# Kernel optimization log

Hardware: AMD Instinct MI355X
Metric: run time of the kernel (lower is better)

Reference implementation:

```python
import jax, jax.numpy as jnp
import numpy as np
from jax import lax

# BinarizedConv2d (threshold=False branch): per-direction binary conv.
# Bits {0,1} map to {-1,+1}; output = 2*A - K where A = #bit-agreements
# between the patch and the filter, K = Cin*kH*kW (the 'offset').
# A = 2*sum(x&w) - sum(x) - sum(w) + K  =>  out = 4*xw - 2*sx - 2*sw + K.

D, H, W, CIN = 64, 32, 32, 128
KH = KW = 3
COUT = 128
PAD = 1


def _binconv(x, w):
    # x: [D,H,W,Cin] bool, w: [D,kH,kW,Cin,Cout] with 0/1 float values
    d, h, wd, c = x.shape
    kh, kw, cout = w.shape[1], w.shape[2], w.shape[4]
    K = c * kh * kw  # offset = in_channels * kH * kW
    xf = jnp.transpose(x.astype(w.dtype), (0, 3, 1, 2))  # [D,C,H,W]
    # im2col: [D, C*kH*kW, Ho, Wo], feature index = c*kH*kW + i*kW + j
    patches = lax.conv_general_dilated_patches(
        xf, (kh, kw), (1, 1), [(PAD, PAD), (PAD, PAD)])
    ho, wo = patches.shape[2], patches.shape[3]
    p = patches.reshape(d, c, kh, kw, ho, wo)
    xw = jnp.einsum('dcijhw,dijco->dhwo', p, w)      # sum(x & w)
    sx = p.sum(axis=(1, 2, 3))                        # [D,Ho,Wo]
    sw = w.sum(axis=(1, 2, 3))                        # [D,Cout]
    return 4.0 * xw - 2.0 * sx[..., None] - 2.0 * sw[:, None, None, :] + K


def setup_inputs() -> dict:
    key = jax.random.key(0)
    kx, kw = jax.random.split(key)
    x = jax.random.bernoulli(kx, 0.5, (D, H, W, CIN))
    w = jax.random.bernoulli(kw, 0.5, (D, KH, KW, CIN, COUT)).astype(jnp.float32)
    return {'x': x, 'w': w}


def reference(x, w):
    return _binconv(x, w)  # [D,Ho,Wo,Cout] signed binary conv values
```

## Files before the change

kernel.cpp:

```cpp
#include <hip/hip_runtime.h>
#include <hip/hip_bf16.h>
#include <stdint.h>


#define D_    64
#define H_    32
#define W_    32
#define CIN_  128
#define COUT_ 128
#define KK_   1152

__global__ __launch_bounds__(256) void pack_x_kernel(const int* __restrict__ x,
                                                     uint4* __restrict__ xb) {
    int gid = blockIdx.x * 256 + threadIdx.x;
    int pos = gid >> 5;
    int c4  = gid & 31;
    const int4* xp = (const int4*)(x + (long)pos * CIN_) + c4;
    int4 v = *xp;
    unsigned long long b0 = __ballot(v.x != 0);
    unsigned long long b1 = __ballot(v.y != 0);
    unsigned long long b2 = __ballot(v.z != 0);
    unsigned long long b3 = __ballot(v.w != 0);
    int lane = threadIdx.x & 63;
    if (lane == 0)
        xb[pos] = make_uint4((unsigned)b0, (unsigned)b1, (unsigned)b2, (unsigned)b3);
    else if (lane == 32)
        xb[pos] = make_uint4((unsigned)(b0 >> 32), (unsigned)(b1 >> 32),
                             (unsigned)(b2 >> 32), (unsigned)(b3 >> 32));
}

__global__ __launch_bounds__(256) void pack_w_kernel(const float* __restrict__ w,
                                                     unsigned* __restrict__ wb) {
    int t    = blockIdx.x * 256 + threadIdx.x;
    int o    = t & 127;
    int rest = t >> 7;
    int k    = rest & 3;
    int dt   = rest >> 2;
    int d    = dt / 9;
    int tap  = dt - d * 9;
    const float* wp = w + (long)dt * (CIN_ * COUT_) + o;
    unsigned m = 0;
#pragma unroll
    for (int j = 0; j < 32; ++j) {
        if (wp[(long)(4 * j + k) * COUT_] != 0.f) m |= 1u << j;
    }
    wb[(((long)d * COUT_ + o) * 9 + tap) * 4 + k] = m;
}

__global__ __launch_bounds__(256) void binconv_kernel(const uint4* __restrict__ xb,
                                                      const uint4* __restrict__ wb,
                                                      float* __restrict__ out) {
    __shared__ uint4 xbt[4][34];

    int bid  = blockIdx.x;
    int d    = bid >> 4;
    int tile = bid & 15;
    int h0   = tile * 2;
    int tid  = threadIdx.x;
    int o    = tid & 127;
    int grp  = tid >> 7;

    if (tid < 4 * 34) {
        int r  = tid / 34;
        int cc = tid - r * 34;
        int hh = h0 - 1 + r;
        int ww = cc - 1;
        uint4 v = make_uint4(0u, 0u, 0u, 0u);
        if (hh >= 0 && hh < H_ && ww >= 0 && ww < W_)
            v = xb[(long)d * (H_ * W_) + hh * W_ + ww];
        xbt[r][cc] = v;
    }

    uint4 wv[9];
    const uint4* wp = wb + (long)(d * COUT_ + o) * 9;
#pragma unroll
    for (int t = 0; t < 9; ++t) wv[t] = wp[t];

    __syncthreads();

    int h = h0 + grp;
    float* op = out + ((long)d * (H_ * W_) + h * W_) * COUT_ + o;

    uint4 ca[3], cb[3], cc_[3];
#pragma unroll
    for (int i = 0; i < 3; ++i) {
        ca[i] = xbt[grp + i][0];
        cb[i] = xbt[grp + i][1];
    }

#pragma unroll
    for (int iw = 0; iw < W_; ++iw) {
#pragma unroll
        for (int i = 0; i < 3; ++i) cc_[i] = xbt[grp + i][iw + 2];
        int pop = 0;
#pragma unroll
        for (int i = 0; i < 3; ++i) {
            uint4 xa;
            uint4 w0 = wv[i * 3 + 0], w1 = wv[i * 3 + 1], w2 = wv[i * 3 + 2];
            xa = ca[i];
            pop += __popc(xa.x ^ w0.x) + __popc(xa.y ^ w0.y)
                 + __popc(xa.z ^ w0.z) + __popc(xa.w ^ w0.w);
            xa = cb[i];
            pop += __popc(xa.x ^ w1.x) + __popc(xa.y ^ w1.y)
                 + __popc(xa.z ^ w1.z) + __popc(xa.w ^ w1.w);
            xa = cc_[i];
            pop += __popc(xa.x ^ w2.x) + __popc(xa.y ^ w2.y)
                 + __popc(xa.z ^ w2.z) + __popc(xa.w ^ w2.w);
        }
        op[(long)iw * COUT_] = (float)(KK_ - 2 * pop);
#pragma unroll
        for (int i = 0; i < 3; ++i) { ca[i] = cb[i]; cb[i] = cc_[i]; }
    }
}

extern "C" void kernel_launch(void* const* d_in, const int* in_sizes, int n_in,
                              void* d_out, int out_size, void* d_ws, size_t ws_size,
                              hipStream_t stream) {
    const int*   x   = (const int*)d_in[0];
    const float* w   = (const float*)d_in[1];
    float*       out = (float*)d_out;

    uint4*    xb = (uint4*)d_ws;
    unsigned* wb = (unsigned*)(xb + (D_ * H_ * W_));

    pack_x_kernel<<<8192, 256, 0, stream>>>(x, xb);
    pack_w_kernel<<<1152, 256, 0, stream>>>(w, wb);
    binconv_kernel<<<1024, 256, 0, stream>>>(xb, (const uint4*)wb, out);
}
```

Before: 128.5 us.

## Fuse x/w bit-packing and binary conv into one kernel

```diff
diff --git a/kernel.cpp b/kernel.cpp
--- a/kernel.cpp
+++ b/kernel.cpp
@@ -1,5 +1,4 @@
 #include <hip/hip_runtime.h>
-#include <hip/hip_bf16.h>
 #include <stdint.h>
 
 
@@ -10,73 +9,71 @@
 #define COUT_ 128
 #define KK_   1152
 
-__global__ __launch_bounds__(256) void pack_x_kernel(const int* __restrict__ x,
-                                                     uint4* __restrict__ xb) {
-    int gid = blockIdx.x * 256 + threadIdx.x;
-    int pos = gid >> 5;
-    int c4  = gid & 31;
-    const int4* xp = (const int4*)(x + (long)pos * CIN_) + c4;
-    int4 v = *xp;
-    unsigned long long b0 = __ballot(v.x != 0);
-    unsigned long long b1 = __ballot(v.y != 0);
-    unsigned long long b2 = __ballot(v.z != 0);
-    unsigned long long b3 = __ballot(v.w != 0);
-    int lane = threadIdx.x & 63;
-    if (lane == 0)
-        xb[pos] = make_uint4((unsigned)b0, (unsigned)b1, (unsigned)b2, (unsigned)b3);
-    else if (lane == 32)
-        xb[pos] = make_uint4((unsigned)(b0 >> 32), (unsigned)(b1 >> 32),
-                             (unsigned)(b2 >> 32), (unsigned)(b3 >> 32));
-}
+__global__ __launch_bounds__(1024) void fused_kernel(const int* __restrict__ x,
+                                                     const float* __restrict__ w,
+                                                     float* __restrict__ out) {
+    __shared__ uint4    xbt[10][34];
+    __shared__ unsigned wt[128][40];
 
-__global__ __launch_bounds__(256) void pack_w_kernel(const float* __restrict__ w,
-                                                     unsigned* __restrict__ wb) {
-    int t    = blockIdx.x * 256 + threadIdx.x;
-    int o    = t & 127;
-    int rest = t >> 7;
-    int k    = rest & 3;
-    int dt   = rest >> 2;
-    int d    = dt / 9;
-    int tap  = dt - d * 9;
-    const float* wp = w + (long)dt * (CIN_ * COUT_) + o;
-    unsigned m = 0;
-#pragma unroll
-    for (int j = 0; j < 32; ++j) {
-        if (wp[(long)(4 * j + k) * COUT_] != 0.f) m |= 1u << j;
-    }
-    wb[(((long)d * COUT_ + o) * 9 + tap) * 4 + k] = m;
-}
+    int tid  = threadIdx.x;
+    int bid  = blockIdx.x;
+    int d    = bid & 63;
+    int tile = bid >> 6;
+    int h0   = tile * 8;
 
-__global__ __launch_bounds__(256) void binconv_kernel(const uint4* __restrict__ xb,
-                                                      const uint4* __restrict__ wb,
-                                                      float* __restrict__ out) {
-    __shared__ uint4 xbt[4][34];
-
-    int bid  = blockIdx.x;
-    int d    = bid >> 4;
-    int tile = bid & 15;
-    int h0   = tile * 2;
-    int tid  = threadIdx.x;
-    int o    = tid & 127;
-    int grp  = tid >> 7;
-
-    if (tid < 4 * 34) {
-        int r  = tid / 34;
-        int cc = tid - r * 34;
-        int hh = h0 - 1 + r;
-        int ww = cc - 1;
-        uint4 v = make_uint4(0u, 0u, 0u, 0u);
-        if (hh >= 0 && hh < H_ && ww >= 0 && ww < W_)
-            v = xb[(long)d * (H_ * W_) + hh * W_ + ww];
-        xbt[r][cc] = v;
+    if (tid < 20) {
+        int r = tid >> 1, c = (tid & 1) ? 33 : 0;
+        xbt[r][c] = make_uint4(0u, 0u, 0u, 0u);
     }
 
-    uint4 wv[9];
-    const uint4* wp = wb + (long)(d * COUT_ + o) * 9;
+    const int* xd = x + (long)d * (H_ * W_ * CIN_);
 #pragma unroll
-    for (int t = 0; t < 9; ++t) wv[t] = wp[t];
+    for (int it = 0; it < 10; ++it) {
+        int t   = tid + it * 1024;
+        int c4  = t & 31;
+        int pl  = t >> 5;
+        int r   = pl >> 5;
+        int col = pl & 31;
+        int hh  = h0 - 1 + r;
+        int4 v = make_int4(0, 0, 0, 0);
+        if (hh >= 0 && hh < H_)
+            v = ((const int4*)(xd + (long)(hh * W_ + col) * CIN_))[c4];
+        unsigned long long b0 = __ballot(v.x != 0);
+        unsigned long long b1 = __ballot(v.y != 0);
+        unsigned long long b2 = __ballot(v.z != 0);
+        unsigned long long b3 = __ballot(v.w != 0);
+        int lane = tid & 63;
+        if (lane == 0)
+            xbt[r][col + 1] = make_uint4((unsigned)b0, (unsigned)b1,
+                                         (unsigned)b2, (unsigned)b3);
+        else if (lane == 32)
+            xbt[r][col + 1] = make_uint4((unsigned)(b0 >> 32), (unsigned)(b1 >> 32),
+                                         (unsigned)(b2 >> 32), (unsigned)(b3 >> 32));
+    }
+
+    const float* wd = w + (long)d * (9 * CIN_ * COUT_);
+    for (int t = tid; t < 4608; t += 1024) {
+        int o    = t & 127;
+        int rest = t >> 7;
+        int tap  = rest >> 2;
+        int k    = rest & 3;
+        const float* wp = wd + (long)tap * (CIN_ * COUT_) + o;
+        unsigned m = 0;
+#pragma unroll
+        for (int j = 0; j < 32; ++j)
+            if (wp[(long)(4 * j + k) * COUT_] != 0.f) m |= 1u << j;
+        wt[o][rest] = m;
+    }
 
     __syncthreads();
+
+    int o   = tid & 127;
+    int grp = tid >> 7;
+
+    uint4 wv[9];
+#pragma unroll
+    for (int t = 0; t < 9; ++t)
+        wv[t] = *(const uint4*)&wt[o][t * 4];
 
     int h = h0 + grp;
     float* op = out + ((long)d * (H_ * W_) + h * W_) * COUT_ + o;
@@ -119,11 +116,7 @@
     const int*   x   = (const int*)d_in[0];
     const float* w   = (const float*)d_in[1];
     float*       out = (float*)d_out;
+    (void)d_ws; (void)ws_size;
 
-    uint4*    xb = (uint4*)d_ws;
-    unsigned* wb = (unsigned*)(xb + (D_ * H_ * W_));
-
-    pack_x_kernel<<<8192, 256, 0, stream>>>(x, xb);
-    pack_w_kernel<<<1152, 256, 0, stream>>>(w, wb);
-    binconv_kernel<<<1024, 256, 0, stream>>>(xb, (const uint4*)wb, out);
+    fused_kernel<<<256, 1024, 0, stream>>>(x, w, out);
 }
```

Result: no change. 128.0 us (-0.4%).

## Merge pack kernels and compute two output rows per thread in binconv

Applied to the files above, without the earlier changes.

```diff
diff --git a/kernel.cpp b/kernel.cpp
--- a/kernel.cpp
+++ b/kernel.cpp
@@ -1,5 +1,4 @@
 #include <hip/hip_runtime.h>
-#include <hip/hip_bf16.h>
 #include <stdint.h>
 
 
@@ -10,57 +9,61 @@
 #define COUT_ 128
 #define KK_   1152
 
-__global__ __launch_bounds__(256) void pack_x_kernel(const int* __restrict__ x,
-                                                     uint4* __restrict__ xb) {
-    int gid = blockIdx.x * 256 + threadIdx.x;
-    int pos = gid >> 5;
-    int c4  = gid & 31;
-    const int4* xp = (const int4*)(x + (long)pos * CIN_) + c4;
-    int4 v = *xp;
-    unsigned long long b0 = __ballot(v.x != 0);
-    unsigned long long b1 = __ballot(v.y != 0);
-    unsigned long long b2 = __ballot(v.z != 0);
-    unsigned long long b3 = __ballot(v.w != 0);
-    int lane = threadIdx.x & 63;
-    if (lane == 0)
-        xb[pos] = make_uint4((unsigned)b0, (unsigned)b1, (unsigned)b2, (unsigned)b3);
-    else if (lane == 32)
-        xb[pos] = make_uint4((unsigned)(b0 >> 32), (unsigned)(b1 >> 32),
-                             (unsigned)(b2 >> 32), (unsigned)(b3 >> 32));
-}
+#define XBLOCKS 8192
+#define WBLOCKS 1152
 
-__global__ __launch_bounds__(256) void pack_w_kernel(const float* __restrict__ w,
-                                                     unsigned* __restrict__ wb) {
-    int t    = blockIdx.x * 256 + threadIdx.x;
-    int o    = t & 127;
-    int rest = t >> 7;
-    int k    = rest & 3;
-    int dt   = rest >> 2;
-    int d    = dt / 9;
-    int tap  = dt - d * 9;
-    const float* wp = w + (long)dt * (CIN_ * COUT_) + o;
-    unsigned m = 0;
+__global__ __launch_bounds__(256) void pack_kernel(const int* __restrict__ x,
+                                                   const float* __restrict__ w,
+                                                   uint4* __restrict__ xb,
+                                                   unsigned* __restrict__ wbw) {
+    int b = blockIdx.x;
+    if (b < XBLOCKS) {
+        int gid = b * 256 + threadIdx.x;
+        int pos = gid >> 5;
+        int c4  = gid & 31;
+        int4 v = ((const int4*)(x + (long)pos * CIN_))[c4];
+        unsigned long long b0 = __ballot(v.x != 0);
+        unsigned long long b1 = __ballot(v.y != 0);
+        unsigned long long b2 = __ballot(v.z != 0);
+        unsigned long long b3 = __ballot(v.w != 0);
+        int lane = threadIdx.x & 63;
+        if (lane == 0)
+            xb[pos] = make_uint4((unsigned)b0, (unsigned)b1,
+                                 (unsigned)b2, (unsigned)b3);
+        else if (lane == 32)
+            xb[pos] = make_uint4((unsigned)(b0 >> 32), (unsigned)(b1 >> 32),
+                                 (unsigned)(b2 >> 32), (unsigned)(b3 >> 32));
+    } else {
+        int t    = (b - XBLOCKS) * 256 + threadIdx.x;
+        int o    = t & 127;
+        int rest = t >> 7;
+        int k    = rest & 3;
+        int dt   = rest >> 2;
+        int d    = dt / 9;
+        int tap  = dt - d * 9;
+        const float* wp = w + (long)dt * (CIN_ * COUT_) + o;
+        unsigned m = 0;
 #pragma unroll
-    for (int j = 0; j < 32; ++j) {
-        if (wp[(long)(4 * j + k) * COUT_] != 0.f) m |= 1u << j;
+        for (int j = 0; j < 32; ++j)
+            if (wp[(long)(4 * j + k) * COUT_] != 0.f) m |= 1u << j;
+        wbw[(((long)d * COUT_ + o) * 9 + tap) * 4 + k] = m;
     }
-    wb[(((long)d * COUT_ + o) * 9 + tap) * 4 + k] = m;
 }
 
 __global__ __launch_bounds__(256) void binconv_kernel(const uint4* __restrict__ xb,
                                                       const uint4* __restrict__ wb,
                                                       float* __restrict__ out) {
-    __shared__ uint4 xbt[4][34];
+    __shared__ uint4 xbt[6][34];
 
     int bid  = blockIdx.x;
-    int d    = bid >> 4;
-    int tile = bid & 15;
-    int h0   = tile * 2;
+    int d    = bid & 63;
+    int tile = bid >> 6;
+    int h0   = tile * 4;
     int tid  = threadIdx.x;
     int o    = tid & 127;
-    int grp  = tid >> 7;
+    int rp   = tid >> 7;
 
-    if (tid < 4 * 34) {
+    if (tid < 6 * 34) {
         int r  = tid / 34;
         int cc = tid - r * 34;
         int hh = h0 - 1 + r;
@@ -78,38 +81,50 @@
 
     __syncthreads();
 
-    int h = h0 + grp;
-    float* op = out + ((long)d * (H_ * W_) + h * W_) * COUT_ + o;
+    int r0 = 2 * rp;
+    int h  = h0 + 2 * rp;
+    float* op0 = out + ((long)d * (H_ * W_) + h * W_) * COUT_ + o;
+    float* op1 = op0 + (long)W_ * COUT_;
 
-    uint4 ca[3], cb[3], cc_[3];
+    uint4 ca[4], cb[4], cc_[4];
 #pragma unroll
-    for (int i = 0; i < 3; ++i) {
-        ca[i] = xbt[grp + i][0];
-        cb[i] = xbt[grp + i][1];
+    for (int i = 0; i < 4; ++i) {
+        ca[i] = xbt[r0 + i][0];
+        cb[i] = xbt[r0 + i][1];
     }
 
 #pragma unroll
     for (int iw = 0; iw < W_; ++iw) {
 #pragma unroll
-        for (int i = 0; i < 3; ++i) cc_[i] = xbt[grp + i][iw + 2];
-        int pop = 0;
+        for (int i = 0; i < 4; ++i) cc_[i] = xbt[r0 + i][iw + 2];
+        int pop0 = 0, pop1 = 0;
 #pragma unroll
-        for (int i = 0; i < 3; ++i) {
+        for (int r = 0; r < 3; ++r) {
+            uint4 wr0 = wv[r * 3 + 0], wr1 = wv[r * 3 + 1], wr2 = wv[r * 3 + 2];
             uint4 xa;
-            uint4 w0 = wv[i * 3 + 0], w1 = wv[i * 3 + 1], w2 = wv[i * 3 + 2];
-            xa = ca[i];
-            pop += __popc(xa.x ^ w0.x) + __popc(xa.y ^ w0.y)
-                 + __popc(xa.z ^ w0.z) + __popc(xa.w ^ w0.w);
-            xa = cb[i];
-            pop += __popc(xa.x ^ w1.x) + __popc(xa.y ^ w1.y)
-                 + __popc(xa.z ^ w1.z) + __popc(xa.w ^ w1.w);
-            xa = cc_[i];
-            pop += __popc(xa.x ^ w2.x) + __popc(xa.y ^ w2.y)
-                 + __popc(xa.z ^ w2.z) + __popc(xa.w ^ w2.w);
+            xa = ca[r];
+            pop0 += __popc(xa.x ^ wr0.x) + __popc(xa.y ^ wr0.y)
+                  + __popc(xa.z ^ wr0.z) + __popc(xa.w ^ wr0.w);
+            xa = ca[r + 1];
+            pop1 += __popc(xa.x ^ wr0.x) + __popc(xa.y ^ wr0.y)
+                  + __popc(xa.z ^ wr0.z) + __popc(xa.w ^ wr0.w);
+            xa = cb[r];
+            pop0 += __popc(xa.x ^ wr1.x) + __popc(xa.y ^ wr1.y)
+                  + __popc(xa.z ^ wr1.z) + __popc(xa.w ^ wr1.w);
+            xa = cb[r + 1];
+            pop1 += __popc(xa.x ^ wr1.x) + __popc(xa.y ^ wr1.y)
+                  + __popc(xa.z ^ wr1.z) + __popc(xa.w ^ wr1.w);
+            xa = cc_[r];
+            pop0 += __popc(xa.x ^ wr2.x) + __popc(xa.y ^ wr2.y)
+                  + __popc(xa.z ^ wr2.z) + __popc(xa.w ^ wr2.w);
+            xa = cc_[r + 1];
+            pop1 += __popc(xa.x ^ wr2.x) + __popc(xa.y ^ wr2.y)
+                  + __popc(xa.z ^ wr2.z) + __popc(xa.w ^ wr2.w);
         }
-        op[(long)iw * COUT_] = (float)(KK_ - 2 * pop);
+        op0[(long)iw * COUT_] = (float)(KK_ - 2 * pop0);
+        op1[(long)iw * COUT_] = (float)(KK_ - 2 * pop1);
 #pragma unroll
-        for (int i = 0; i < 3; ++i) { ca[i] = cb[i]; cb[i] = cc_[i]; }
+        for (int i = 0; i < 4; ++i) { ca[i] = cb[i]; cb[i] = cc_[i]; }
     }
 }
 
@@ -120,10 +135,9 @@
     const float* w   = (const float*)d_in[1];
     float*       out = (float*)d_out;
 
-    uint4*    xb = (uint4*)d_ws;
-    unsigned* wb = (unsigned*)(xb + (D_ * H_ * W_));
+    uint4*    xb  = (uint4*)d_ws;
+    unsigned* wbw = (unsigned*)(xb + (D_ * H_ * W_));
 
-    pack_x_kernel<<<8192, 256, 0, stream>>>(x, xb);
-    pack_w_kernel<<<1152, 256, 0, stream>>>(w, wb);
-    binconv_kernel<<<1024, 256, 0, stream>>>(xb, (const uint4*)wb, out);
+    pack_kernel<<<XBLOCKS + WBLOCKS, 256, 0, stream>>>(x, w, xb, wbw);
+    binconv_kernel<<<512, 256, 0, stream>>>(xb, (const uint4*)wbw, out);
 }
```

After: 129.8 us. Within noise of the previous version (+1.0%).
